# Performance work log

Hardware: AMD Instinct MI355X
Metric: run time of the kernel (lower is better)

The kernel has to match this reference:

```python
import jax, jax.numpy as jnp
import numpy as np
from jax import lax

B, N, S, NSAMPLE = 8, 4096, 1024, 32
RADIUS = 0.2
EPS = 1e-5
IN_CH = 64
MLP = [64, 64, 128]


def _fps(xyz, npoint):
    # farthest point sampling; deterministic start at index 0 (torch uses a random start)
    b, n, _ = xyz.shape
    bidx = jnp.arange(b)

    def step(carry, _):
        distance, farthest = carry
        centroid = xyz[bidx, farthest][:, None, :]            # [B,1,3]
        d = jnp.sum((xyz - centroid) ** 2, axis=-1)           # [B,N]
        distance = jnp.minimum(distance, d)
        nxt = jnp.argmax(distance, axis=-1).astype(jnp.int32)
        return (distance, nxt), farthest

    init = (jnp.full((b, n), 1e10, dtype=xyz.dtype), jnp.zeros((b,), jnp.int32))
    _, idxs = lax.scan(step, init, None, length=npoint)
    return idxs.T                                             # [B,npoint]


def _index_points(p, idx):
    # p: [B,N,C], idx: [B,...] -> [B,...,C]
    return jax.vmap(lambda pp, ii: pp[ii])(p, idx)


def _square_distance(src, dst):
    # src [B,S,3], dst [B,N,3] -> [B,S,N]
    d = -2.0 * jnp.einsum('bsc,bnc->bsn', src, dst)
    d += jnp.sum(src ** 2, -1)[:, :, None]
    d += jnp.sum(dst ** 2, -1)[:, None, :]
    return d


def _query_ball(radius, nsample, xyz, new_xyz):
    n = xyz.shape[1]
    sqr = _square_distance(new_xyz, xyz)                      # [B,S,N]
    gidx = jnp.where(sqr > radius ** 2, n, jnp.arange(n, dtype=jnp.int32))
    gidx = jnp.sort(gidx, axis=-1)[:, :, :nsample]            # [B,S,nsample]
    first = gidx[:, :, :1]
    return jnp.where(gidx == n, first, gidx)


def setup_inputs() -> dict:
    key = jax.random.key(0)
    ks = jax.random.split(key, 8)
    inp = {
        'xyz': jax.random.uniform(ks[0], (B, N, 3), jnp.float32),
        'points': jax.random.normal(ks[1], (B, N, IN_CH), jnp.float32),
    }
    last = IN_CH + 3
    for i, out_c in enumerate(MLP):
        scale = 1.0 / np.sqrt(last)
        inp[f'w{i}'] = jax.random.normal(ks[2 + i], (out_c, last), jnp.float32) * scale
        inp[f'b{i}'] = jnp.zeros((out_c,), jnp.float32)
        inp[f'g{i}'] = jnp.ones((out_c,), jnp.float32)
        inp[f'be{i}'] = jnp.zeros((out_c,), jnp.float32)
        last = out_c
    return inp


def _forward(xyz, points, params):
    fps_idx = _fps(xyz, S)
    new_xyz = _index_points(xyz, fps_idx)                     # [B,S,3]
    idx = _query_ball(RADIUS, NSAMPLE, xyz, new_xyz)          # [B,S,n]
    grouped_xyz = _index_points(xyz, idx) - new_xyz[:, :, None, :]
    h = jnp.concatenate([grouped_xyz, _index_points(points, idx)], axis=-1)  # [B,S,n,67]
    for (w, b, g, be) in params:
        h = jnp.einsum('bsnc,oc->bsno', h, w) + b             # 1x1 conv
        mu = jnp.mean(h, axis=(0, 1, 2))
        var = jnp.var(h, axis=(0, 1, 2))                      # training-mode batch norm
        h = jax.nn.relu((h - mu) * lax.rsqrt(var + EPS) * g + be)
    new_points = jnp.max(h, axis=2)                           # [B,S,Cout]
    return new_xyz, jnp.transpose(new_points, (0, 2, 1))      # [B,Cout,S] like torch


def reference(xyz, points, w0, b0, g0, be0, w1, b1, g1, be1, w2, b2, g2, be2):
    params = [(w0, b0, g0, be0), (w1, b1, g1, be1), (w2, b2, g2, be2)]
    return _forward(xyz, points, params)
```

## Files before the change

### kernel.cpp

```cpp
#include <hip/hip_runtime.h>
#include <stdint.h>

#define NB 8
#define NPTS 4096
#define NS 1024
#define NK 32
#define NROWS (NB*NS*NK)
#define R2 0.04f
#define NCOPY 32

typedef __attribute__((ext_vector_type(8))) short bf16x8;
typedef __attribute__((ext_vector_type(4))) float f32x4;
typedef __attribute__((ext_vector_type(2))) float f32x2;

__device__ __forceinline__ float bf2f(uint16_t u){
    uint32_t v = ((uint32_t)u) << 16;
    return __uint_as_float(v);
}
__device__ __forceinline__ uint16_t f2bf(float f){
    uint32_t u = __float_as_uint(f);
    uint32_t r = (u + 0x7FFFu + ((u >> 16) & 1u)) >> 16;
    return (uint16_t)r;
}
__device__ __forceinline__ bf16x8 load_bf8(const uint16_t* p){
    return *reinterpret_cast<const bf16x8*>(p);
}

__device__ __forceinline__ void publish_cent(float* cent, int cell,
                                             float cx, float cy, float cz){
    f32x4 v; v[0] = cx; v[1] = cy; v[2] = cz; v[3] = 1.0f;
    unsigned long long a = (unsigned long long)(uintptr_t)(cent + (size_t)cell*4);
    asm volatile("global_store_dwordx4 %0, %1, off sc0 sc1"
                 :: "v"(a), "v"(v) : "memory");
}
__device__ __forceinline__ f32x4 wait_cent(const float* cent, int cell){
    const uint32_t* wp = (const uint32_t*)(cent + (size_t)cell*4) + 3;
    while (__hip_atomic_load(wp, __ATOMIC_RELAXED, __HIP_MEMORY_SCOPE_AGENT)
           != 0x3F800000u)
        __builtin_amdgcn_s_sleep(32);
    f32x4 r;
    unsigned long long a = (unsigned long long)(uintptr_t)(cent + (size_t)cell*4);
    asm volatile("global_load_dwordx4 %0, %1, off sc0 sc1\n\ts_waitcnt vmcnt(0)"
                 : "=v"(r) : "v"(a) : "memory");
    return r;
}

#define DPPMAX64(key, ctrl, rmask)                                             \
    {                                                                          \
        uint32_t _lo = (uint32_t)(key), _hi = (uint32_t)((key) >> 32);         \
        uint32_t _olo = (uint32_t)__builtin_amdgcn_update_dpp(                 \
            0, (int)_lo, (ctrl), (rmask), 0xf, true);                          \
        uint32_t _ohi = (uint32_t)__builtin_amdgcn_update_dpp(                 \
            0, (int)_hi, (ctrl), (rmask), 0xf, true);                          \
        unsigned long long _o = (((unsigned long long)_ohi) << 32) | _olo;     \
        key = (_o > (key)) ? _o : (key);                                       \
    }

struct FpsSh {
    float LX[NPTS], LY[NPTS], LZ[NPTS];
    f32x4 SC[NS];
    alignas(16) unsigned long long cand[2][4];
};
struct WrkSh {
    float S_s[16][64], S_q[16][64];
    int   idxL[2][NK];
    f32x4 Lc[2];
};
union MegaSh { FpsSh f; WrkSh w; char force_one_block_per_cu[86016]; };

#define FT 16
__global__ __launch_bounds__(256) void mega_kernel(const float* __restrict__ xyz,
                                                   const float* __restrict__ pts,
                                                   const uint16_t* __restrict__ w0b,
                                                   const float* __restrict__ b0,
                                                   uint16_t* __restrict__ z0,
                                                   double* __restrict__ accumOut,
                                                   float* __restrict__ cent,
                                                   float* __restrict__ out_newxyz){
    __shared__ MegaSh sh;
    const int t = threadIdx.x;

    if (blockIdx.x < NB){
        const int b = blockIdx.x;
        const float* base = xyz + (size_t)b * (NPTS*3);
        f32x2 px2[FT/2], py2[FT/2], pz2[FT/2], pd2[FT/2];
#pragma unroll
        for (int j = 0; j < FT/2; ++j){
            int i = t*FT + 2*j;
            float x0 = base[i*3+0], y0 = base[i*3+1], z0c = base[i*3+2];
            float x1 = base[i*3+3], y1 = base[i*3+4], z1c = base[i*3+5];
            px2[j] = (f32x2){x0, x1};
            py2[j] = (f32x2){y0, y1};
            pz2[j] = (f32x2){z0c, z1c};
            pd2[j] = (f32x2){1e10f, 1e10f};
            sh.f.LX[i]=x0; sh.f.LY[i]=y0; sh.f.LZ[i]=z0c;
            sh.f.LX[i+1]=x1; sh.f.LY[i+1]=y1; sh.f.LZ[i+1]=z1c;
        }
        __syncthreads();
        int cur = 0;
        const int wave = t >> 6, lane = t & 63;
        for (int s = 0; s < NS; ++s){
            float cx = sh.f.LX[cur], cy = sh.f.LY[cur], cz = sh.f.LZ[cur];
            if (t == 0){
                sh.f.SC[s] = (f32x4){cx, cy, cz, 0.f};
                publish_cent(cent, b*NS + s, cx, cy, cz);
            }
            f32x2 ncx = (f32x2){-cx, -cx};
            f32x2 ncy = (f32x2){-cy, -cy};
            f32x2 ncz = (f32x2){-cz, -cz};
            float bestd = -1.0f; int besti = 0;
#pragma unroll
            for (int j = 0; j < FT/2; ++j){
                f32x2 d2;
                {
#pragma clang fp contract(off)
                    f32x2 dx = px2[j] + ncx;
                    f32x2 dy = py2[j] + ncy;
                    f32x2 dz = pz2[j] + ncz;
                    f32x2 xx = dx*dx, yy = dy*dy, zz = dz*dz;
                    d2 = (xx + yy) + zz;
                }
                f32x2 nd;
                nd.x = fminf(pd2[j].x, d2.x);
                nd.y = fminf(pd2[j].y, d2.y);
                pd2[j] = nd;
                if (nd.x > bestd){ bestd = nd.x; besti = t*FT + 2*j; }
                if (nd.y > bestd){ bestd = nd.y; besti = t*FT + 2*j + 1; }
            }
            unsigned long long key =
                (((unsigned long long)__float_as_uint(bestd)) << 32) |
                (unsigned long long)(~(unsigned)besti);
            DPPMAX64(key, 0x111, 0xf);
            DPPMAX64(key, 0x112, 0xf);
            DPPMAX64(key, 0x114, 0xf);
            DPPMAX64(key, 0x118, 0xf);
            DPPMAX64(key, 0x142, 0xa);
            DPPMAX64(key, 0x143, 0xc);
            int p = s & 1;
            if (lane == 63) sh.f.cand[p][wave] = key;
            __syncthreads();
            ulonglong2 c01 = *reinterpret_cast<const ulonglong2*>(&sh.f.cand[p][0]);
            ulonglong2 c23 = *reinterpret_cast<const ulonglong2*>(&sh.f.cand[p][2]);
            unsigned long long m01 = (c01.x > c01.y) ? c01.x : c01.y;
            unsigned long long m23 = (c23.x > c23.y) ? c23.x : c23.y;
            unsigned long long km  = (m01 > m23) ? m01 : m23;
            cur = (int)(~(uint32_t)km);
        }
        __syncthreads();
        for (int i = t; i < NS; i += 256){
            f32x4 c = sh.f.SC[i];
            float* o = out_newxyz + ((size_t)b*NS + i)*3;
            o[0] = c[0]; o[1] = c[1]; o[2] = c[2];
        }
    } else {
        const int w = (int)blockIdx.x - NB;
        const int stile = w >> 3;
        const int b = w & 7;
        const int wave = t >> 6, lane = t & 63;
        const int q = lane >> 4, l16 = lane & 15;

        bf16x8 Bf[4][3];
#pragma unroll
        for (int nt = 0; nt < 4; ++nt)
#pragma unroll
            for (int s = 0; s < 3; ++s)
                Bf[nt][s] = load_bf8(w0b + (nt*16 + l16)*96 + s*32 + q*8);

        if (t == 0){
            sh.w.Lc[0] = wait_cent(cent, b*NS + stile*2 + 0);
            sh.w.Lc[1] = wait_cent(cent, b*NS + stile*2 + 1);
        }
        __syncthreads();

        if (wave < 2){
            f32x4 qc = sh.w.Lc[wave];
            float qx = qc[0], qy = qc[1], qz = qc[2];
            float qn = qx*qx;
            qn = fmaf(qy, qy, qn);
            qn = fmaf(qz, qz, qn);
            const float* base = xyz + (size_t)b * (NPTS*3);
            int cnt = 0, first = 0;
            for (int c0 = 0; c0 < NPTS; c0 += 64){
                int i = c0 + lane;
                float x = base[i*3+0], y = base[i*3+1], z = base[i*3+2];
                float xn = x*x;
                xn = fmaf(y, y, xn);
                xn = fmaf(z, z, xn);
                float dot = qx*x;
                dot = fmaf(qy, y, dot);
                dot = fmaf(qz, z, dot);
                float d;
                {
#pragma clang fp contract(off)
                    d = -2.0f * dot;
                    d = d + qn;
                    d = d + xn;
                }
                bool in = !(d > R2);
                unsigned long long m = __ballot(in);
                if (in){
                    int rank = __popcll(m & ((1ull << lane) - 1ull));
                    int pos = cnt + rank;
                    if (pos < NK) sh.w.idxL[wave][pos] = i;
                }
                if (cnt == 0 && m) first = c0 + (__ffsll((unsigned long long)m) - 1);
                cnt += __popcll(m);
                if (cnt >= NK) break;
            }
            if (cnt < NK){
                for (int p = cnt + lane; p < NK; p += 64) sh.w.idxL[wave][p] = first;
            }
        }
        __syncthreads();

        const int rowbase = (b*NS + stile*2)*NK;
        const int r0 = rowbase + wave*16;
        const int cell = wave >> 1;
        const int sample = (wave & 1)*16 + l16;
        const int id = sh.w.idxL[cell][sample];
        const float* prow = pts + (((size_t)b << 12) + id)*64;
        const float* xr   = xyz + (((size_t)b << 12) + id)*3;
        f32x4 qc = sh.w.Lc[cell];
        float d0 = xr[0]-qc[0], d1 = xr[1]-qc[1], d2 = xr[2]-qc[2];

        f32x4 acc[4];
#pragma unroll
        for (int nt = 0; nt < 4; ++nt) acc[nt] = (f32x4){0.f,0.f,0.f,0.f};

#pragma unroll
        for (int s = 0; s < 3; ++s){
            const int k0 = s*32 + q*8;
            bf16x8 a;
#pragma unroll
            for (int j = 0; j < 8; ++j){
                int k = k0 + j;
                float v = (k < 3) ? ((k == 0) ? d0 : ((k == 1) ? d1 : d2))
                                  : ((k < 67) ? prow[k-3] : 0.f);
                a[j] = (short)f2bf(v);
            }
#pragma unroll
            for (int nt = 0; nt < 4; ++nt)
                acc[nt] = __builtin_amdgcn_mfma_f32_16x16x32_bf16(a, Bf[nt][s], acc[nt], 0, 0, 0);
        }
#pragma unroll
        for (int nt = 0; nt < 4; ++nt){
            int c = nt*16 + l16;
            float bb = b0[c];
            float sps = 0.f, spq = 0.f;
#pragma unroll
            for (int reg = 0; reg < 4; ++reg){
                int rr = r0 + q*4 + reg;
                float h = acc[nt][reg] + bb;
                sps += h;
                spq = fmaf(h, h, spq);
                z0[(size_t)rr*64 + c] = f2bf(h);
            }
            sh.w.S_s[wave*4 + q][c] = sps;
            sh.w.S_q[wave*4 + q][c] = spq;
        }
        __syncthreads();
        if (t < 64){
            double ss = 0.0, sq = 0.0;
#pragma unroll
            for (int i = 0; i < 16; ++i){ ss += (double)sh.w.S_s[i][t]; sq += (double)sh.w.S_q[i][t]; }
            int cp = blockIdx.x & (NCOPY-1);
            atomicAdd(&accumOut[cp*256 + t], ss);
            atomicAdd(&accumOut[cp*256 + 128 + t], sq);
        }
    }
}

__global__ void prep_kernel(const float* __restrict__ w0, const float* __restrict__ w1,
                            const float* __restrict__ w2, uint16_t* __restrict__ w0b,
                            uint16_t* __restrict__ w1b, uint16_t* __restrict__ w2b,
                            double* __restrict__ accumAll, float* __restrict__ cent){
    int t = blockIdx.x*256 + threadIdx.x;
    int stride = gridDim.x*256;
    for (int i = t; i < 3*NCOPY*256; i += stride) accumAll[i] = 0.0;
    for (int i = t; i < NB*NS; i += stride)
        ((f32x4*)cent)[i] = (f32x4){0.f, 0.f, 0.f, 0.f};
    for (int i = t; i < 64*96; i += stride){
        int n = i/96, c = i%96;
        w0b[i] = (c < 67) ? f2bf(w0[n*67 + c]) : (uint16_t)0;
    }
    for (int i = t; i < 64*64; i += stride)  w1b[i] = f2bf(w1[i]);
    for (int i = t; i < 128*64; i += stride) w2b[i] = f2bf(w2[i]);
}

__global__ __launch_bounds__(256) void layer1_mfma(const uint16_t* __restrict__ zin,
                                                   const double* __restrict__ accumIn,
                                                   const float* __restrict__ g,
                                                   const float* __restrict__ be,
                                                   const uint16_t* __restrict__ wb,
                                                   const float* __restrict__ bias,
                                                   uint16_t* __restrict__ zout,
                                                   double* __restrict__ accumOut){
    constexpr int NT = 4;
    __shared__ float sc_l[64], sh_l[64];
    __shared__ float S_s[16][64], S_q[16][64];
    const int t = threadIdx.x;
    if (t < 64){
        double s = 0.0, qq = 0.0;
#pragma unroll
        for (int cp = 0; cp < NCOPY; ++cp){
            s  += accumIn[cp*256 + t];
            qq += accumIn[cp*256 + 128 + t];
        }
        double mean = s / (double)NROWS;
        double var  = qq / (double)NROWS - mean*mean;
        double rs = 1.0 / sqrt(var + 1e-5);
        double scv = (double)g[t] * rs;
        sc_l[t] = (float)scv;
        sh_l[t] = (float)((double)be[t] - mean*scv);
    }
    __syncthreads();

    const int wave = t >> 6, lane = t & 63;
    const int q = lane >> 4, l16 = lane & 15;
    const int r0 = blockIdx.x*64 + wave*16;

    bf16x8 Bf[NT][2];
#pragma unroll
    for (int nt = 0; nt < NT; ++nt)
#pragma unroll
        for (int s = 0; s < 2; ++s)
            Bf[nt][s] = load_bf8(wb + (nt*16 + l16)*64 + s*32 + q*8);

    float sc[2][8], sh[2][8];
#pragma unroll
    for (int s = 0; s < 2; ++s)
#pragma unroll
        for (int j = 0; j < 8; ++j){
            sc[s][j] = sc_l[s*32 + q*8 + j];
            sh[s][j] = sh_l[s*32 + q*8 + j];
        }

    f32x4 acc[NT];
#pragma unroll
    for (int nt = 0; nt < NT; ++nt) acc[nt] = (f32x4){0.f,0.f,0.f,0.f};

    const uint16_t* zr = zin + (size_t)(r0 + l16)*64;
#pragma unroll
    for (int s = 0; s < 2; ++s){
        uint4 u = *reinterpret_cast<const uint4*>(zr + s*32 + q*8);
        float h[8];
        h[0] = bf2f((uint16_t)(u.x & 0xFFFF)); h[1] = bf2f((uint16_t)(u.x >> 16));
        h[2] = bf2f((uint16_t)(u.y & 0xFFFF)); h[3] = bf2f((uint16_t)(u.y >> 16));
        h[4] = bf2f((uint16_t)(u.z & 0xFFFF)); h[5] = bf2f((uint16_t)(u.z >> 16));
        h[6] = bf2f((uint16_t)(u.w & 0xFFFF)); h[7] = bf2f((uint16_t)(u.w >> 16));
        bf16x8 a;
#pragma unroll
        for (int j = 0; j < 8; ++j){
            float v = fmaxf(fmaf(h[j], sc[s][j], sh[s][j]), 0.f);
            a[j] = (short)f2bf(v);
        }
#pragma unroll
        for (int nt = 0; nt < NT; ++nt)
            acc[nt] = __builtin_amdgcn_mfma_f32_16x16x32_bf16(a, Bf[nt][s], acc[nt], 0, 0, 0);
    }
#pragma unroll
    for (int nt = 0; nt < NT; ++nt){
        int c = nt*16 + l16;
        float bb = bias[c];
        float sps = 0.f, spq = 0.f;
#pragma unroll
        for (int reg = 0; reg < 4; ++reg){
            int rr = r0 + q*4 + reg;
            float h = acc[nt][reg] + bb;
            sps += h;
            spq = fmaf(h, h, spq);
            zout[(size_t)rr*64 + c] = f2bf(h);
        }
        S_s[wave*4 + q][c] = sps;
        S_q[wave*4 + q][c] = spq;
    }
    __syncthreads();
    if (t < 64){
        double ss = 0.0, sq = 0.0;
#pragma unroll
        for (int i = 0; i < 16; ++i){ ss += (double)S_s[i][t]; sq += (double)S_q[i][t]; }
        int cp = blockIdx.x & (NCOPY-1);
        atomicAdd(&accumOut[cp*256 + t], ss);
        atomicAdd(&accumOut[cp*256 + 128 + t], sq);
    }
}

__global__ __launch_bounds__(256) void layer2_mfma(const uint16_t* __restrict__ zin,
                                                   const double* __restrict__ accumIn,
                                                   const float* __restrict__ g,
                                                   const float* __restrict__ be,
                                                   const uint16_t* __restrict__ wb,
                                                   const float* __restrict__ bias,
                                                   float2* __restrict__ pool,
                                                   double* __restrict__ accumOut){
    constexpr int NT = 8;
    __shared__ float sc_l[64], sh_l[64];
    __shared__ float S_s[16][128], S_q[16][128];
    __shared__ float P_mx[16][128], P_mn[16][128];
    const int t = threadIdx.x;
    if (t < 64){
        double s = 0.0, qq = 0.0;
#pragma unroll
        for (int cp = 0; cp < NCOPY; ++cp){
            s  += accumIn[cp*256 + t];
            qq += accumIn[cp*256 + 128 + t];
        }
        double mean = s / (double)NROWS;
        double var  = qq / (double)NROWS - mean*mean;
        double rs = 1.0 / sqrt(var + 1e-5);
        double scv = (double)g[t] * rs;
        sc_l[t] = (float)scv;
        sh_l[t] = (float)((double)be[t] - mean*scv);
    }
    __syncthreads();

    const int wave = t >> 6, lane = t & 63;
    const int q = lane >> 4, l16 = lane & 15;
    const int r0 = blockIdx.x*64 + wave*16;

    bf16x8 Bf[NT][2];
#pragma unroll
    for (int nt = 0; nt < NT; ++nt)
#pragma unroll
        for (int s = 0; s < 2; ++s)
            Bf[nt][s] = load_bf8(wb + (nt*16 + l16)*64 + s*32 + q*8);

    float sc[2][8], sh[2][8];
#pragma unroll
    for (int s = 0; s < 2; ++s)
#pragma unroll
        for (int j = 0; j < 8; ++j){
            sc[s][j] = sc_l[s*32 + q*8 + j];
            sh[s][j] = sh_l[s*32 + q*8 + j];
        }

    f32x4 acc[NT];
#pragma unroll
    for (int nt = 0; nt < NT; ++nt) acc[nt] = (f32x4){0.f,0.f,0.f,0.f};

    const uint16_t* zr = zin + (size_t)(r0 + l16)*64;
#pragma unroll
    for (int s = 0; s < 2; ++s){
        uint4 u = *reinterpret_cast<const uint4*>(zr + s*32 + q*8);
        float h[8];
        h[0] = bf2f((uint16_t)(u.x & 0xFFFF)); h[1] = bf2f((uint16_t)(u.x >> 16));
        h[2] = bf2f((uint16_t)(u.y & 0xFFFF)); h[3] = bf2f((uint16_t)(u.y >> 16));
        h[4] = bf2f((uint16_t)(u.z & 0xFFFF)); h[5] = bf2f((uint16_t)(u.z >> 16));
        h[6] = bf2f((uint16_t)(u.w & 0xFFFF)); h[7] = bf2f((uint16_t)(u.w >> 16));
        bf16x8 a;
#pragma unroll
        for (int j = 0; j < 8; ++j){
            float v = fmaxf(fmaf(h[j], sc[s][j], sh[s][j]), 0.f);
            a[j] = (short)f2bf(v);
        }
#pragma unroll
        for (int nt = 0; nt < NT; ++nt)
            acc[nt] = __builtin_amdgcn_mfma_f32_16x16x32_bf16(a, Bf[nt][s], acc[nt], 0, 0, 0);
    }
#pragma unroll
    for (int nt = 0; nt < NT; ++nt){
        int c = nt*16 + l16;
        float bb = bias[c];
        float sps = 0.f, spq = 0.f;
        float mx = -1e30f, mn = 1e30f;
#pragma unroll
        for (int reg = 0; reg < 4; ++reg){
            float h = acc[nt][reg] + bb;
            sps += h;
            spq = fmaf(h, h, spq);
            mx = fmaxf(mx, h);
            mn = fminf(mn, h);
        }
        S_s[wave*4 + q][c] = sps;
        S_q[wave*4 + q][c] = spq;
        P_mx[wave*4 + q][c] = mx;
        P_mn[wave*4 + q][c] = mn;
    }
    __syncthreads();
    if (t < 128){
        double ss = 0.0, sq = 0.0;
#pragma unroll
        for (int i = 0; i < 16; ++i){ ss += (double)S_s[i][t]; sq += (double)S_q[i][t]; }
        int cp = blockIdx.x & (NCOPY-1);
        atomicAdd(&accumOut[cp*256 + t], ss);
        atomicAdd(&accumOut[cp*256 + 128 + t], sq);
    }
    {
        int gidx = t >> 7;
        int c = t & 127;
        float mx = -1e30f, mn = 1e30f;
#pragma unroll
        for (int i = 0; i < 8; ++i){
            mx = fmaxf(mx, P_mx[gidx*8 + i][c]);
            mn = fminf(mn, P_mn[gidx*8 + i][c]);
        }
        pool[(size_t)(blockIdx.x*2 + gidx)*128 + c] = make_float2(mx, mn);
    }
}

__global__ __launch_bounds__(256) void final_kernel(const float2* __restrict__ pool,
                                                    const double* __restrict__ accumIn,
                                                    const float* __restrict__ g,
                                                    const float* __restrict__ be,
                                                    float* __restrict__ out){
    __shared__ float sc_l[128], sh_l[128];
    const int t0 = threadIdx.x;
    if (t0 < 128){
        double s = 0.0, qq = 0.0;
#pragma unroll
        for (int cp = 0; cp < NCOPY; ++cp){
            s  += accumIn[cp*256 + t0];
            qq += accumIn[cp*256 + 128 + t0];
        }
        double mean = s / (double)NROWS;
        double var  = qq / (double)NROWS - mean*mean;
        double rs = 1.0 / sqrt(var + 1e-5);
        double scv = (double)g[t0] * rs;
        sc_l[t0] = (float)scv;
        sh_l[t0] = (float)((double)be[t0] - mean*scv);
    }
    __syncthreads();

    int t = blockIdx.x*256 + threadIdx.x;
    int o = t & 127;
    int s = (t >> 7) & 1023;
    int b = t >> 17;
    float2 p = pool[t];
    float sc = sc_l[o], sh = sh_l[o];
    float zsel = (sc >= 0.f) ? p.x : p.y;
    float y = fmaxf(fmaf(zsel, sc, sh), 0.f);
    out[24576 + ((size_t)b << 17) + ((size_t)o << 10) + s] = y;
}

extern "C" void kernel_launch(void* const* d_in, const int* in_sizes, int n_in,
                              void* d_out, int out_size, void* d_ws, size_t ws_size,
                              hipStream_t stream) {
    const float* xyz = (const float*)d_in[0];
    const float* pts = (const float*)d_in[1];
    const float* w0  = (const float*)d_in[2];
    const float* b0  = (const float*)d_in[3];
    const float* g0  = (const float*)d_in[4];
    const float* be0 = (const float*)d_in[5];
    const float* w1  = (const float*)d_in[6];
    const float* b1  = (const float*)d_in[7];
    const float* g1  = (const float*)d_in[8];
    const float* be1 = (const float*)d_in[9];
    const float* w2  = (const float*)d_in[10];
    const float* b2  = (const float*)d_in[11];
    const float* g2  = (const float*)d_in[12];
    const float* be2 = (const float*)d_in[13];
    float* out = (float*)d_out;

    char* ws = (char*)d_ws;
    double*   accum0 = (double*)(ws + 0);
    double*   accum1 = (double*)(ws + 65536);
    double*   accum2 = (double*)(ws + 131072);
    uint16_t* w0b    = (uint16_t*)(ws + 196608);
    uint16_t* w1b    = (uint16_t*)(ws + 208896);
    uint16_t* w2b    = (uint16_t*)(ws + 217088);
    uint16_t* z0     = (uint16_t*)(ws + 262144);
    uint16_t* z1     = (uint16_t*)(ws + 33816576);
    float2*   pool   = (float2*)  (ws + 67371008);
    float*    cent   = (float*)   (ws + 75759616);

    prep_kernel<<<32, 256, 0, stream>>>(w0, w1, w2, w0b, w1b, w2b, accum0, cent);
    mega_kernel<<<NB + 4096, 256, 0, stream>>>(xyz, pts, w0b, b0, z0, accum0, cent, out);
    layer1_mfma<<<4096, 256, 0, stream>>>(z0, accum0, g0, be0, w1b, b1, z1, accum1);
    layer2_mfma<<<4096, 256, 0, stream>>>(z1, accum1, g1, be1, w2b, b2, pool, accum2);
    final_kernel<<<4096, 256, 0, stream>>>(pool, accum2, g2, be2, out);
}
```

Before: 817.4 us.

## Compute batch-norm scale/shift once via last-block ticket instead of per block

Each producer kernel now counts finished blocks with an atomic ticket, and the last block reduces the 32 double-precision accumulator copies into per-channel scale/shift arrays. Consumer kernels then load those precomputed values instead of every one of 4096 blocks redoing the 32-way double reduction. The FPS loop also spreads the centroid publish and the shared-memory store across different waves and replaces __syncthreads with a raw lgkmcnt wait plus barrier. In exchange there is extra fence and atomic traffic at every block end, and correctness now depends on ticket reset and memory ordering.

Result: slower. 1.726 ms (+111.2%).

```diff
diff --git a/kernel.cpp b/kernel.cpp
--- a/kernel.cpp
+++ b/kernel.cpp
@@ -25,6 +25,8 @@
 __device__ __forceinline__ bf16x8 load_bf8(const uint16_t* p){
     return *reinterpret_cast<const bf16x8*>(p);
 }
+
+#define BAR_LGKM() asm volatile("s_waitcnt lgkmcnt(0)\n\ts_barrier" ::: "memory")
 
 __device__ __forceinline__ void publish_cent(float* cent, int cell,
                                              float cx, float cy, float cz){
@@ -43,6 +45,25 @@
     asm volatile("global_load_dwordx4 %0, %1, off sc0 sc1\n\ts_waitcnt vmcnt(0)"
                  : "=v"(r) : "v"(a) : "memory");
     return r;
+}
+
+__device__ __forceinline__ void compute_scsh(const double* accum, const float* g,
+                                             const float* be, int nch,
+                                             float* scsh, int t){
+    if (t < nch){
+        double s = 0.0, qq = 0.0;
+#pragma unroll
+        for (int cp = 0; cp < NCOPY; ++cp){
+            s  += __hip_atomic_load(&accum[cp*256 + t],       __ATOMIC_RELAXED, __HIP_MEMORY_SCOPE_AGENT);
+            qq += __hip_atomic_load(&accum[cp*256 + 128 + t], __ATOMIC_RELAXED, __HIP_MEMORY_SCOPE_AGENT);
+        }
+        double mean = s / (double)NROWS;
+        double var  = qq / (double)NROWS - mean*mean;
+        double rs = 1.0 / sqrt(var + 1e-5);
+        double scv = (double)g[t] * rs;
+        scsh[t]       = (float)scv;
+        scsh[nch + t] = (float)((double)be[t] - mean*scv);
+    }
 }
 
 #define DPPMAX64(key, ctrl, rmask)                                             \
@@ -76,8 +97,13 @@
                                                    uint16_t* __restrict__ z0,
                                                    double* __restrict__ accumOut,
                                                    float* __restrict__ cent,
-                                                   float* __restrict__ out_newxyz){
+                                                   float* __restrict__ out_newxyz,
+                                                   const float* __restrict__ g0,
+                                                   const float* __restrict__ be0,
+                                                   float* __restrict__ scsh0,
+                                                   int* __restrict__ ticket0){
     __shared__ MegaSh sh;
+    __shared__ int s_last;
     const int t = threadIdx.x;
 
     if (blockIdx.x < NB){
@@ -101,10 +127,8 @@
         const int wave = t >> 6, lane = t & 63;
         for (int s = 0; s < NS; ++s){
             float cx = sh.f.LX[cur], cy = sh.f.LY[cur], cz = sh.f.LZ[cur];
-            if (t == 0){
-                sh.f.SC[s] = (f32x4){cx, cy, cz, 0.f};
-                publish_cent(cent, b*NS + s, cx, cy, cz);
-            }
+            if (t == 64) publish_cent(cent, b*NS + s, cx, cy, cz);
+            if (t == 192) sh.f.SC[s] = (f32x4){cx, cy, cz, 0.f};
             f32x2 ncx = (f32x2){-cx, -cx};
             f32x2 ncy = (f32x2){-cy, -cy};
             f32x2 ncz = (f32x2){-cz, -cz};
@@ -138,7 +162,7 @@
             DPPMAX64(key, 0x143, 0xc);
             int p = s & 1;
             if (lane == 63) sh.f.cand[p][wave] = key;
-            __syncthreads();
+            BAR_LGKM();
             ulonglong2 c01 = *reinterpret_cast<const ulonglong2*>(&sh.f.cand[p][0]);
             ulonglong2 c23 = *reinterpret_cast<const ulonglong2*>(&sh.f.cand[p][2]);
             unsigned long long m01 = (c01.x > c01.y) ? c01.x : c01.y;
@@ -267,15 +291,27 @@
             atomicAdd(&accumOut[cp*256 + t], ss);
             atomicAdd(&accumOut[cp*256 + 128 + t], sq);
         }
+        __threadfence();
+        if (t == 0){
+            int done = __hip_atomic_fetch_add(ticket0, 1, __ATOMIC_ACQ_REL, __HIP_MEMORY_SCOPE_AGENT);
+            s_last = (done == 4096 - 1);
+        }
+        __syncthreads();
+        if (s_last){
+            __threadfence();
+            compute_scsh(accumOut, g0, be0, 64, scsh0, t);
+        }
     }
 }
 
 __global__ void prep_kernel(const float* __restrict__ w0, const float* __restrict__ w1,
                             const float* __restrict__ w2, uint16_t* __restrict__ w0b,
                             uint16_t* __restrict__ w1b, uint16_t* __restrict__ w2b,
-                            double* __restrict__ accumAll, float* __restrict__ cent){
+                            double* __restrict__ accumAll, float* __restrict__ cent,
+                            int* __restrict__ tickets){
     int t = blockIdx.x*256 + threadIdx.x;
     int stride = gridDim.x*256;
+    if (t < 16) tickets[t] = 0;
     for (int i = t; i < 3*NCOPY*256; i += stride) accumAll[i] = 0.0;
     for (int i = t; i < NB*NS; i += stride)
         ((f32x4*)cent)[i] = (f32x4){0.f, 0.f, 0.f, 0.f};
@@ -288,31 +324,21 @@
 }
 
 __global__ __launch_bounds__(256) void layer1_mfma(const uint16_t* __restrict__ zin,
-                                                   const double* __restrict__ accumIn,
-                                                   const float* __restrict__ g,
-                                                   const float* __restrict__ be,
+                                                   const float* __restrict__ scsh_in,
                                                    const uint16_t* __restrict__ wb,
                                                    const float* __restrict__ bias,
                                                    uint16_t* __restrict__ zout,
-                                                   double* __restrict__ accumOut){
+                                                   double* __restrict__ accumOut,
+                                                   const float* __restrict__ g1,
+                                                   const float* __restrict__ be1,
+                                                   float* __restrict__ scsh_out,
+                                                   int* __restrict__ ticket){
     constexpr int NT = 4;
     __shared__ float sc_l[64], sh_l[64];
     __shared__ float S_s[16][64], S_q[16][64];
+    __shared__ int s_last;
     const int t = threadIdx.x;
-    if (t < 64){
-        double s = 0.0, qq = 0.0;
-#pragma unroll
-        for (int cp = 0; cp < NCOPY; ++cp){
-            s  += accumIn[cp*256 + t];
-            qq += accumIn[cp*256 + 128 + t];
-        }
-        double mean = s / (double)NROWS;
-        double var  = qq / (double)NROWS - mean*mean;
-        double rs = 1.0 / sqrt(var + 1e-5);
-        double scv = (double)g[t] * rs;
-        sc_l[t] = (float)scv;
-        sh_l[t] = (float)((double)be[t] - mean*scv);
-    }
+    if (t < 64){ sc_l[t] = scsh_in[t]; sh_l[t] = scsh_in[64 + t]; }
     __syncthreads();
 
     const int wave = t >> 6, lane = t & 63;
@@ -383,35 +409,35 @@
         atomicAdd(&accumOut[cp*256 + t], ss);
         atomicAdd(&accumOut[cp*256 + 128 + t], sq);
     }
+    __threadfence();
+    if (t == 0){
+        int done = __hip_atomic_fetch_add(ticket, 1, __ATOMIC_ACQ_REL, __HIP_MEMORY_SCOPE_AGENT);
+        s_last = (done == 4096 - 1);
+    }
+    __syncthreads();
+    if (s_last){
+        __threadfence();
+        compute_scsh(accumOut, g1, be1, 64, scsh_out, t);
+    }
 }
 
 __global__ __launch_bounds__(256) void layer2_mfma(const uint16_t* __restrict__ zin,
-                                                   const double* __restrict__ accumIn,
-                                                   const float* __restrict__ g,
-                                                   const float* __restrict__ be,
+                                                   const float* __restrict__ scsh_in,
                                                    const uint16_t* __restrict__ wb,
                                                    const float* __restrict__ bias,
                                                    float2* __restrict__ pool,
-                                                   double* __restrict__ accumOut){
+                                                   double* __restrict__ accumOut,
+                                                   const float* __restrict__ g2,
+                                                   const float* __restrict__ be2,
+                                                   float* __restrict__ scsh_out,
+                                                   int* __restrict__ ticket){
     constexpr int NT = 8;
     __shared__ float sc_l[64], sh_l[64];
     __shared__ float S_s[16][128], S_q[16][128];
     __shared__ float P_mx[16][128], P_mn[16][128];
+    __shared__ int s_last;
     const int t = threadIdx.x;
-    if (t < 64){
-        double s = 0.0, qq = 0.0;
-#pragma unroll
-        for (int cp = 0; cp < NCOPY; ++cp){
-            s  += accumIn[cp*256 + t];
-            qq += accumIn[cp*256 + 128 + t];
-        }
-        double mean = s / (double)NROWS;
-        double var  = qq / (double)NROWS - mean*mean;
-        double rs = 1.0 / sqrt(var + 1e-5);
-        double scv = (double)g[t] * rs;
-        sc_l[t] = (float)scv;
-        sh_l[t] = (float)((double)be[t] - mean*scv);
-    }
+    if (t < 64){ sc_l[t] = scsh_in[t]; sh_l[t] = scsh_in[64 + t]; }
     __syncthreads();
 
     const int wave = t >> 6, lane = t & 63;
@@ -496,29 +522,24 @@
         }
         pool[(size_t)(blockIdx.x*2 + gidx)*128 + c] = make_float2(mx, mn);
     }
+    __threadfence();
+    if (t == 0){
+        int done = __hip_atomic_fetch_add(ticket, 1, __ATOMIC_ACQ_REL, __HIP_MEMORY_SCOPE_AGENT);
+        s_last = (done == 4096 - 1);
+    }
+    __syncthreads();
+    if (s_last){
+        __threadfence();
+        compute_scsh(accumOut, g2, be2, 128, scsh_out, t);
+    }
 }
 
 __global__ __launch_bounds__(256) void final_kernel(const float2* __restrict__ pool,
-                                                    const double* __restrict__ accumIn,
-                                                    const float* __restrict__ g,
-                                                    const float* __restrict__ be,
+                                                    const float* __restrict__ scsh_in,
                                                     float* __restrict__ out){
     __shared__ float sc_l[128], sh_l[128];
     const int t0 = threadIdx.x;
-    if (t0 < 128){
-        double s = 0.0, qq = 0.0;
-#pragma unroll
-        for (int cp = 0; cp < NCOPY; ++cp){
-            s  += accumIn[cp*256 + t0];
-            qq += accumIn[cp*256 + 128 + t0];
-        }
-        double mean = s / (double)NROWS;
-        double var  = qq / (double)NROWS - mean*mean;
-        double rs = 1.0 / sqrt(var + 1e-5);
-        double scv = (double)g[t0] * rs;
-        sc_l[t0] = (float)scv;
-        sh_l[t0] = (float)((double)be[t0] - mean*scv);
-    }
+    if (t0 < 128){ sc_l[t0] = scsh_in[t0]; sh_l[t0] = scsh_in[128 + t0]; }
     __syncthreads();
 
     int t = blockIdx.x*256 + threadIdx.x;
@@ -562,10 +583,17 @@
     uint16_t* z1     = (uint16_t*)(ws + 33816576);
     float2*   pool   = (float2*)  (ws + 67371008);
     float*    cent   = (float*)   (ws + 75759616);
-
-    prep_kernel<<<32, 256, 0, stream>>>(w0, w1, w2, w0b, w1b, w2b, accum0, cent);
-    mega_kernel<<<NB + 4096, 256, 0, stream>>>(xyz, pts, w0b, b0, z0, accum0, cent, out);
-    layer1_mfma<<<4096, 256, 0, stream>>>(z0, accum0, g0, be0, w1b, b1, z1, accum1);
-    layer2_mfma<<<4096, 256, 0, stream>>>(z1, accum1, g1, be1, w2b, b2, pool, accum2);
-    final_kernel<<<4096, 256, 0, stream>>>(pool, accum2, g2, be2, out);
-}
+    float*    scsh0  = (float*)   (ws + 75890688);
+    float*    scsh1  = (float*)   (ws + 75891200);
+    float*    scsh2  = (float*)   (ws + 75891712);
+    int*      tickets= (int*)     (ws + 75892736);
+
+    prep_kernel<<<32, 256, 0, stream>>>(w0, w1, w2, w0b, w1b, w2b, accum0, cent, tickets);
+    mega_kernel<<<NB + 4096, 256, 0, stream>>>(xyz, pts, w0b, b0, z0, accum0, cent, out,
+                                               g0, be0, scsh0, &tickets[0]);
+    layer1_mfma<<<4096, 256, 0, stream>>>(z0, scsh0, w1b, b1, z1, accum1,
+                                          g1, be1, scsh1, &tickets[1]);
+    layer2_mfma<<<4096, 256, 0, stream>>>(z1, scsh1, w2b, b2, pool, accum2,
+                                          g2, be2, scsh2, &tickets[2]);
+    final_kernel<<<4096, 256, 0, stream>>>(pool, scsh2, out);
+}
```

## Process multiple row tiles per block in MLP kernels and trim FPS barrier

Applied to the files above, without the earlier changes.

Layer1, layer2 and final kernels now have each block loop over four 64-row tiles, with a quarter as many blocks. This amortizes the per-block BN-statistics reduction over NCOPY doubles, the weight fragment loads, and the fp64 atomics across more work. In the FPS loop, the centroid publish and the shared-memory store move to threads in different waves, and __syncthreads is replaced by an explicit lgkmcnt wait plus s_barrier, to shorten the serial per-step critical path. The trade-off is fewer blocks in flight, which may reduce latency hiding, and extra barriers inside the tile loop.

After: 804.9 us. About the same (-1.5%).

```diff
diff --git a/kernel.cpp b/kernel.cpp
--- a/kernel.cpp
+++ b/kernel.cpp
@@ -25,6 +25,8 @@
 __device__ __forceinline__ bf16x8 load_bf8(const uint16_t* p){
     return *reinterpret_cast<const bf16x8*>(p);
 }
+
+#define BAR_LGKM() asm volatile("s_waitcnt lgkmcnt(0)\n\ts_barrier" ::: "memory")
 
 __device__ __forceinline__ void publish_cent(float* cent, int cell,
                                              float cx, float cy, float cz){
@@ -101,10 +103,8 @@
         const int wave = t >> 6, lane = t & 63;
         for (int s = 0; s < NS; ++s){
             float cx = sh.f.LX[cur], cy = sh.f.LY[cur], cz = sh.f.LZ[cur];
-            if (t == 0){
-                sh.f.SC[s] = (f32x4){cx, cy, cz, 0.f};
-                publish_cent(cent, b*NS + s, cx, cy, cz);
-            }
+            if (t == 64) publish_cent(cent, b*NS + s, cx, cy, cz);
+            if (t == 192) sh.f.SC[s] = (f32x4){cx, cy, cz, 0.f};
             f32x2 ncx = (f32x2){-cx, -cx};
             f32x2 ncy = (f32x2){-cy, -cy};
             f32x2 ncz = (f32x2){-cz, -cz};
@@ -138,7 +138,7 @@
             DPPMAX64(key, 0x143, 0xc);
             int p = s & 1;
             if (lane == 63) sh.f.cand[p][wave] = key;
-            __syncthreads();
+            BAR_LGKM();
             ulonglong2 c01 = *reinterpret_cast<const ulonglong2*>(&sh.f.cand[p][0]);
             ulonglong2 c23 = *reinterpret_cast<const ulonglong2*>(&sh.f.cand[p][2]);
             unsigned long long m01 = (c01.x > c01.y) ? c01.x : c01.y;
@@ -296,6 +296,7 @@
                                                    uint16_t* __restrict__ zout,
                                                    double* __restrict__ accumOut){
     constexpr int NT = 4;
+    constexpr int TPB = 4;
     __shared__ float sc_l[64], sh_l[64];
     __shared__ float S_s[16][64], S_q[16][64];
     const int t = threadIdx.x;
@@ -317,7 +318,6 @@
 
     const int wave = t >> 6, lane = t & 63;
     const int q = lane >> 4, l16 = lane & 15;
-    const int r0 = blockIdx.x*64 + wave*16;
 
     bf16x8 Bf[NT][2];
 #pragma unroll
@@ -335,53 +335,61 @@
             sh[s][j] = sh_l[s*32 + q*8 + j];
         }
 
-    f32x4 acc[NT];
-#pragma unroll
-    for (int nt = 0; nt < NT; ++nt) acc[nt] = (f32x4){0.f,0.f,0.f,0.f};
-
-    const uint16_t* zr = zin + (size_t)(r0 + l16)*64;
-#pragma unroll
-    for (int s = 0; s < 2; ++s){
-        uint4 u = *reinterpret_cast<const uint4*>(zr + s*32 + q*8);
-        float h[8];
-        h[0] = bf2f((uint16_t)(u.x & 0xFFFF)); h[1] = bf2f((uint16_t)(u.x >> 16));
-        h[2] = bf2f((uint16_t)(u.y & 0xFFFF)); h[3] = bf2f((uint16_t)(u.y >> 16));
-        h[4] = bf2f((uint16_t)(u.z & 0xFFFF)); h[5] = bf2f((uint16_t)(u.z >> 16));
-        h[6] = bf2f((uint16_t)(u.w & 0xFFFF)); h[7] = bf2f((uint16_t)(u.w >> 16));
-        bf16x8 a;
-#pragma unroll
-        for (int j = 0; j < 8; ++j){
-            float v = fmaxf(fmaf(h[j], sc[s][j], sh[s][j]), 0.f);
-            a[j] = (short)f2bf(v);
-        }
-#pragma unroll
-        for (int nt = 0; nt < NT; ++nt)
-            acc[nt] = __builtin_amdgcn_mfma_f32_16x16x32_bf16(a, Bf[nt][s], acc[nt], 0, 0, 0);
-    }
-#pragma unroll
-    for (int nt = 0; nt < NT; ++nt){
-        int c = nt*16 + l16;
-        float bb = bias[c];
-        float sps = 0.f, spq = 0.f;
-#pragma unroll
-        for (int reg = 0; reg < 4; ++reg){
-            int rr = r0 + q*4 + reg;
-            float h = acc[nt][reg] + bb;
-            sps += h;
-            spq = fmaf(h, h, spq);
-            zout[(size_t)rr*64 + c] = f2bf(h);
-        }
-        S_s[wave*4 + q][c] = sps;
-        S_q[wave*4 + q][c] = spq;
-    }
-    __syncthreads();
+    double accS = 0.0, accQ = 0.0;
+
+    for (int tile = 0; tile < TPB; ++tile){
+        const int r0 = (blockIdx.x*TPB + tile)*64 + wave*16;
+
+        f32x4 acc[NT];
+#pragma unroll
+        for (int nt = 0; nt < NT; ++nt) acc[nt] = (f32x4){0.f,0.f,0.f,0.f};
+
+        const uint16_t* zr = zin + (size_t)(r0 + l16)*64;
+#pragma unroll
+        for (int s = 0; s < 2; ++s){
+            uint4 u = *reinterpret_cast<const uint4*>(zr + s*32 + q*8);
+            float h[8];
+            h[0] = bf2f((uint16_t)(u.x & 0xFFFF)); h[1] = bf2f((uint16_t)(u.x >> 16));
+            h[2] = bf2f((uint16_t)(u.y & 0xFFFF)); h[3] = bf2f((uint16_t)(u.y >> 16));
+            h[4] = bf2f((uint16_t)(u.z & 0xFFFF)); h[5] = bf2f((uint16_t)(u.z >> 16));
+            h[6] = bf2f((uint16_t)(u.w & 0xFFFF)); h[7] = bf2f((uint16_t)(u.w >> 16));
+            bf16x8 a;
+#pragma unroll
+            for (int j = 0; j < 8; ++j){
+                float v = fmaxf(fmaf(h[j], sc[s][j], sh[s][j]), 0.f);
+                a[j] = (short)f2bf(v);
+            }
+#pragma unroll
+            for (int nt = 0; nt < NT; ++nt)
+                acc[nt] = __builtin_amdgcn_mfma_f32_16x16x32_bf16(a, Bf[nt][s], acc[nt], 0, 0, 0);
+        }
+#pragma unroll
+        for (int nt = 0; nt < NT; ++nt){
+            int c = nt*16 + l16;
+            float bb = bias[c];
+            float sps = 0.f, spq = 0.f;
+#pragma unroll
+            for (int reg = 0; reg < 4; ++reg){
+                int rr = r0 + q*4 + reg;
+                float h = acc[nt][reg] + bb;
+                sps += h;
+                spq = fmaf(h, h, spq);
+                zout[(size_t)rr*64 + c] = f2bf(h);
+            }
+            S_s[wave*4 + q][c] = sps;
+            S_q[wave*4 + q][c] = spq;
+        }
+        __syncthreads();
+        if (t < 64){
+#pragma unroll
+            for (int i = 0; i < 16; ++i){ accS += (double)S_s[i][t]; accQ += (double)S_q[i][t]; }
+        }
+        __syncthreads();
+    }
     if (t < 64){
-        double ss = 0.0, sq = 0.0;
-#pragma unroll
-        for (int i = 0; i < 16; ++i){ ss += (double)S_s[i][t]; sq += (double)S_q[i][t]; }
         int cp = blockIdx.x & (NCOPY-1);
-        atomicAdd(&accumOut[cp*256 + t], ss);
-        atomicAdd(&accumOut[cp*256 + 128 + t], sq);
+        atomicAdd(&accumOut[cp*256 + t], accS);
+        atomicAdd(&accumOut[cp*256 + 128 + t], accQ);
     }
 }
 
@@ -394,6 +402,7 @@
                                                    float2* __restrict__ pool,
                                                    double* __restrict__ accumOut){
     constexpr int NT = 8;
+    constexpr int TPB = 4;
     __shared__ float sc_l[64], sh_l[64];
     __shared__ float S_s[16][128], S_q[16][128];
     __shared__ float P_mx[16][128], P_mn[16][128];
@@ -416,7 +425,6 @@
 
     const int wave = t >> 6, lane = t & 63;
     const int q = lane >> 4, l16 = lane & 15;
-    const int r0 = blockIdx.x*64 + wave*16;
 
     bf16x8 Bf[NT][2];
 #pragma unroll
@@ -434,67 +442,75 @@
             sh[s][j] = sh_l[s*32 + q*8 + j];
         }
 
-    f32x4 acc[NT];
-#pragma unroll
-    for (int nt = 0; nt < NT; ++nt) acc[nt] = (f32x4){0.f,0.f,0.f,0.f};
-
-    const uint16_t* zr = zin + (size_t)(r0 + l16)*64;
-#pragma unroll
-    for (int s = 0; s < 2; ++s){
-        uint4 u = *reinterpret_cast<const uint4*>(zr + s*32 + q*8);
-        float h[8];
-        h[0] = bf2f((uint16_t)(u.x & 0xFFFF)); h[1] = bf2f((uint16_t)(u.x >> 16));
-        h[2] = bf2f((uint16_t)(u.y & 0xFFFF)); h[3] = bf2f((uint16_t)(u.y >> 16));
-        h[4] = bf2f((uint16_t)(u.z & 0xFFFF)); h[5] = bf2f((uint16_t)(u.z >> 16));
-        h[6] = bf2f((uint16_t)(u.w & 0xFFFF)); h[7] = bf2f((uint16_t)(u.w >> 16));
-        bf16x8 a;
-#pragma unroll
-        for (int j = 0; j < 8; ++j){
-            float v = fmaxf(fmaf(h[j], sc[s][j], sh[s][j]), 0.f);
-            a[j] = (short)f2bf(v);
-        }
-#pragma unroll
-        for (int nt = 0; nt < NT; ++nt)
-            acc[nt] = __builtin_amdgcn_mfma_f32_16x16x32_bf16(a, Bf[nt][s], acc[nt], 0, 0, 0);
-    }
-#pragma unroll
-    for (int nt = 0; nt < NT; ++nt){
-        int c = nt*16 + l16;
-        float bb = bias[c];
-        float sps = 0.f, spq = 0.f;
-        float mx = -1e30f, mn = 1e30f;
-#pragma unroll
-        for (int reg = 0; reg < 4; ++reg){
-            float h = acc[nt][reg] + bb;
-            sps += h;
-            spq = fmaf(h, h, spq);
-            mx = fmaxf(mx, h);
-            mn = fminf(mn, h);
-        }
-        S_s[wave*4 + q][c] = sps;
-        S_q[wave*4 + q][c] = spq;
-        P_mx[wave*4 + q][c] = mx;
-        P_mn[wave*4 + q][c] = mn;
-    }
-    __syncthreads();
+    double accS = 0.0, accQ = 0.0;
+
+    for (int tile = 0; tile < TPB; ++tile){
+        const int r0 = (blockIdx.x*TPB + tile)*64 + wave*16;
+
+        f32x4 acc[NT];
+#pragma unroll
+        for (int nt = 0; nt < NT; ++nt) acc[nt] = (f32x4){0.f,0.f,0.f,0.f};
+
+        const uint16_t* zr = zin + (size_t)(r0 + l16)*64;
+#pragma unroll
+        for (int s = 0; s < 2; ++s){
+            uint4 u = *reinterpret_cast<const uint4*>(zr + s*32 + q*8);
+            float h[8];
+            h[0] = bf2f((uint16_t)(u.x & 0xFFFF)); h[1] = bf2f((uint16_t)(u.x >> 16));
+            h[2] = bf2f((uint16_t)(u.y & 0xFFFF)); h[3] = bf2f((uint16_t)(u.y >> 16));
+            h[4] = bf2f((uint16_t)(u.z & 0xFFFF)); h[5] = bf2f((uint16_t)(u.z >> 16));
+            h[6] = bf2f((uint16_t)(u.w & 0xFFFF)); h[7] = bf2f((uint16_t)(u.w >> 16));
+            bf16x8 a;
+#pragma unroll
+            for (int j = 0; j < 8; ++j){
+                float v = fmaxf(fmaf(h[j], sc[s][j], sh[s][j]), 0.f);
+                a[j] = (short)f2bf(v);
+            }
+#pragma unroll
+            for (int nt = 0; nt < NT; ++nt)
+                acc[nt] = __builtin_amdgcn_mfma_f32_16x16x32_bf16(a, Bf[nt][s], acc[nt], 0, 0, 0);
+        }
+#pragma unroll
+        for (int nt = 0; nt < NT; ++nt){
+            int c = nt*16 + l16;
+            float bb = bias[c];
+            float sps = 0.f, spq = 0.f;
+            float mx = -1e30f, mn = 1e30f;
+#pragma unroll
+            for (int reg = 0; reg < 4; ++reg){
+                float h = acc[nt][reg] + bb;
+                sps += h;
+                spq = fmaf(h, h, spq);
+                mx = fmaxf(mx, h);
+                mn = fminf(mn, h);
+            }
+            S_s[wave*4 + q][c] = sps;
+            S_q[wave*4 + q][c] = spq;
+            P_mx[wave*4 + q][c] = mx;
+            P_mn[wave*4 + q][c] = mn;
+        }
+        __syncthreads();
+        if (t < 128){
+#pragma unroll
+            for (int i = 0; i < 16; ++i){ accS += (double)S_s[i][t]; accQ += (double)S_q[i][t]; }
+        }
+        {
+            int gidx = t >> 7;
+            int c = t & 127;
+            float mx = -1e30f, mn = 1e30f;
+#pragma unroll
+            for (int i = 0; i < 8; ++i){
+                mx = fmaxf(mx, P_mx[gidx*8 + i][c]);
+                mn = fminf(mn, P_mn[gidx*8 + i][c]);
+            }
+            pool[(size_t)((blockIdx.x*TPB + tile)*2 + gidx)*128 + c] = make_float2(mx, mn);
+        }
+        __syncthreads();
+    }
     if (t < 128){
-        double ss = 0.0, sq = 0.0;
-#pragma unroll
-        for (int i = 0; i < 16; ++i){ ss += (double)S_s[i][t]; sq += (double)S_q[i][t]; }
         int cp = blockIdx.x & (NCOPY-1);
-        atomicAdd(&accumOut[cp*256 + t], ss);
-        atomicAdd(&accumOut[cp*256 + 128 + t], sq);
-    }
-    {
-        int gidx = t >> 7;
-        int c = t & 127;
-        float mx = -1e30f, mn = 1e30f;
-#pragma unroll
-        for (int i = 0; i < 8; ++i){
-            mx = fmaxf(mx, P_mx[gidx*8 + i][c]);
-            mn = fminf(mn, P_mn[gidx*8 + i][c]);
-        }
-        pool[(size_t)(blockIdx.x*2 + gidx)*128 + c] = make_float2(mx, mn);
+        atomicAdd(&accumOut[cp*256 + t], accS);
+        atomicAdd(&accumOut[cp*256 + 128 + t], accQ);
     }
 }
 
@@ -521,15 +537,18 @@
     }
     __syncthreads();
 
-    int t = blockIdx.x*256 + threadIdx.x;
-    int o = t & 127;
-    int s = (t >> 7) & 1023;
-    int b = t >> 17;
-    float2 p = pool[t];
-    float sc = sc_l[o], sh = sh_l[o];
-    float zsel = (sc >= 0.f) ? p.x : p.y;
-    float y = fmaxf(fmaf(zsel, sc, sh), 0.f);
-    out[24576 + ((size_t)b << 17) + ((size_t)o << 10) + s] = y;
+#pragma unroll
+    for (int it = 0; it < 4; ++it){
+        int t = blockIdx.x*1024 + it*256 + threadIdx.x;
+        int o = t & 127;
+        int s = (t >> 7) & 1023;
+        int b = t >> 17;
+        float2 p = pool[t];
+        float sc = sc_l[o], sh = sh_l[o];
+        float zsel = (sc >= 0.f) ? p.x : p.y;
+        float y = fmaxf(fmaf(zsel, sc, sh), 0.f);
+        out[24576 + ((size_t)b << 17) + ((size_t)o << 10) + s] = y;
+    }
 }
 
 extern "C" void kernel_launch(void* const* d_in, const int* in_sizes, int n_in,
@@ -565,7 +584,7 @@
 
     prep_kernel<<<32, 256, 0, stream>>>(w0, w1, w2, w0b, w1b, w2b, accum0, cent);
     mega_kernel<<<NB + 4096, 256, 0, stream>>>(xyz, pts, w0b, b0, z0, accum0, cent, out);
-    layer1_mfma<<<4096, 256, 0, stream>>>(z0, accum0, g0, be0, w1b, b1, z1, accum1);
-    layer2_mfma<<<4096, 256, 0, stream>>>(z1, accum1, g1, be1, w2b, b2, pool, accum2);
-    final_kernel<<<4096, 256, 0, stream>>>(pool, accum2, g2, be2, out);
-}
+    layer1_mfma<<<1024, 256, 0, stream>>>(z0, accum0, g0, be0, w1b, b1, z1, accum1);
+    layer2_mfma<<<1024, 256, 0, stream>>>(z1, accum1, g1, be1, w2b, b2, pool, accum2);
+    final_kernel<<<1024, 256, 0, stream>>>(pool, accum2, g2, be2, out);
+}
```
